# Optimization experiments

Hardware: AMD Instinct MI355X
Metric: run time of the kernel (lower is better)

## Reference

```python
import jax, jax.numpy as jnp
import numpy as np

HEADS = 32


def _conv1x1(x, w, b):
    # x: (B, Cin, H, W); w: (Cout, Cin); 1x1 conv == per-pixel GEMM
    return jnp.einsum('bchw,oc->bohw', x, w) + b[None, :, None, None]


def _grid_sample2d_zeros(value, grid):
    # value: (N, C, H, W); grid: (N, H, W, 2), normalized coords in [-1, 1],
    # grid[..., 0] = x (width axis), grid[..., 1] = y (height axis).
    # Bilinear, align_corners=True, zeros padding applied per dimension.
    N, C, H, W = value.shape
    ix = (grid[..., 0] + 1.0) * (W - 1) * 0.5
    iy = (grid[..., 1] + 1.0) * (H - 1) * 0.5
    x0 = jnp.floor(ix)
    y0 = jnp.floor(iy)
    dx = ix - x0  # (N, H, W)
    dy = iy - y0
    x0i = x0.astype(jnp.int32)
    y0i = y0.astype(jnp.int32)
    x1i = x0i + 1
    y1i = y0i + 1

    def gather(yi, xi):
        valid = ((xi >= 0) & (xi < W) & (yi >= 0) & (yi < H))
        xc = jnp.clip(xi, 0, W - 1)
        yc = jnp.clip(yi, 0, H - 1)
        g = jax.vmap(lambda v, y, x: v[:, y, x])(value, yc, xc)  # (N, C, H, W)
        return g * valid[:, None, :, :].astype(value.dtype)

    out = (gather(y0i, x0i) * ((1.0 - dx) * (1.0 - dy))[:, None]
           + gather(y0i, x1i) * (dx * (1.0 - dy))[:, None]
           + gather(y1i, x0i) * ((1.0 - dx) * dy)[:, None]
           + gather(y1i, x1i) * (dx * dy)[:, None])
    return out


def _base_grid(H, W, dtype):
    ys = jnp.linspace(-1.0, 1.0, H, dtype=dtype)
    xs = jnp.linspace(-1.0, 1.0, W, dtype=dtype)
    gy, gx = jnp.meshgrid(ys, xs, indexing='ij')
    return jnp.stack([gx, gy], axis=-1)  # (H, W, 2)


def setup_inputs() -> dict:
    key = jax.random.key(0)
    k = jax.random.split(key, 8)
    B, Cin, Cout, H, W = 4, 256, 256, 128, 128
    u = jax.random.normal(k[0], (B, Cin, H, W), dtype=jnp.float32)
    s_in = 1.0 / np.sqrt(Cin)
    s_out = 1.0 / np.sqrt(Cout)
    w1 = jax.random.normal(k[1], (Cout, Cin), dtype=jnp.float32) * s_in
    b1 = jax.random.normal(k[2], (Cout,), dtype=jnp.float32) * 0.01
    w2 = jax.random.normal(k[3], (2 * HEADS, Cout), dtype=jnp.float32) * (0.1 * s_out)
    b2 = jax.random.normal(k[4], (2 * HEADS,), dtype=jnp.float32) * 0.01
    wv = jax.random.normal(k[5], (Cout, Cin), dtype=jnp.float32) * s_in
    bv = jax.random.normal(k[6], (Cout,), dtype=jnp.float32) * 0.01
    return {"u": u, "w1": w1, "b1": b1, "w2": w2, "b2": b2, "wv": wv, "bv": bv}


def reference(u, w1, b1, w2, b2, wv, bv):
    B, Cin, H, W = u.shape
    # flow_head: 1x1 conv -> ReLU -> 1x1 conv producing n_dims*heads channels
    h = jax.nn.relu(_conv1x1(u, w1, b1))
    flow = _conv1x1(h, w2, b2)          # (B, heads*2, H, W)
    value = _conv1x1(u, wv, bv)         # (B, Cout, H, W)
    Ci = value.shape[1] // HEADS
    # 'B (heads dir) H W -> (B heads) H W dir'
    flow = flow.reshape(B, HEADS, 2, H, W).transpose(0, 1, 3, 4, 2)
    flow = flow.reshape(B * HEADS, H, W, 2)
    # 'B (heads C_i) H W -> (B heads) C_i H W'
    value = value.reshape(B * HEADS, Ci, H, W)
    grid = _base_grid(H, W, u.dtype)[None] + flow  # (B*heads, H, W, 2)
    warp = _grid_sample2d_zeros(value, grid)       # (B*heads, Ci, H, W)
    # '(B heads) C_i H W -> B (heads C_i) H W'
    return warp.reshape(B, HEADS * Ci, H, W)
```

## Files before the change

kernel.cpp:

```cpp
#include <hip/hip_runtime.h>
#include <cstddef>

#define HW 16384

typedef short s8v __attribute__((ext_vector_type(8)));
typedef short s4v __attribute__((ext_vector_type(4)));
typedef float f4v __attribute__((ext_vector_type(4)));

__device__ inline short f2b(float x) {
    union { float f; unsigned u; } v; v.f = x;
    unsigned r = v.u + 0x7fff + ((v.u >> 16) & 1);
    return (short)(r >> 16);
}
__device__ inline float b2f(short h) {
    union { unsigned u; float f; } v;
    v.u = ((unsigned)(unsigned short)h) << 16;
    return v.f;
}

__device__ inline void bar_lgkm() {
    asm volatile("s_waitcnt lgkmcnt(0)\n\ts_barrier" ::: "memory");
}

__global__ __launch_bounds__(256) void k_prep_w(
    const float* __restrict__ w1, const float* __restrict__ wv,
    const float* __restrict__ w2,
    short* __restrict__ Wthi, short* __restrict__ Wtlo,
    short* __restrict__ w2thi, short* __restrict__ w2tlo)
{
    int tid = blockIdx.x * 256 + threadIdx.x;
    if (tid < 131072) {
        int c = tid >> 14, r = tid & 16383, ch = r >> 5, kk = r & 31;
        float f = (ch < 256) ? w1[ch * 256 + c * 32 + kk]
                             : wv[(ch - 256) * 256 + c * 32 + kk];
        short hi = f2b(f);
        Wthi[tid] = hi;
        if (ch < 256) Wtlo[(c * 256 + ch) * 32 + kk] = f2b(f - b2f(hi));
    } else {
        int o = tid - 131072;
        int c = o >> 11, r = o & 2047, dir = r >> 5, kk = r & 31;
        float f = w2[dir * 256 + c * 32 + kk];
        short hi = f2b(f);
        w2thi[o] = hi;
        w2tlo[o] = f2b(f - b2f(hi));
    }
}

__global__ __launch_bounds__(256, 2) void k_mega(
    const float* __restrict__ u,
    const short* __restrict__ Wthi, const short* __restrict__ Wtlo,
    const short* __restrict__ w2thi, const short* __restrict__ w2tlo,
    const float* __restrict__ b1, const float* __restrict__ bv,
    const float* __restrict__ b2,
    unsigned short* __restrict__ vbuf, float* __restrict__ flow)
{
    __shared__ __attribute__((aligned(16))) char smem[69632];
    short* T1h = (short*)smem;
    short* T1l = T1h + 4352;
    short* T2h = (short*)(smem + 17408);
    short* T2l = T2h + 4608;
    short* vt  = (short*)smem;
    short* hhi = (short*)smem;
    short* hlo = (short*)(smem + 34816);

    const int t = threadIdx.x;
    const int l = t & 63;
    const int w = t >> 6;
    const int lr = l & 15;
    const int quad = l >> 4;
    const int quad8 = quad * 8;
    const int pt = blockIdx.x * 64;
    const int b  = pt >> 14;
    const int p0 = pt & 16383;
    const float* ub = u + (size_t)b * 256 * HW + p0;
    const int pxB = 16 * w + lr;

    f4v acc_h[4][4], acc_v[4][4];
    #pragma unroll
    for (int i = 0; i < 4; ++i)
        #pragma unroll
        for (int j = 0; j < 4; ++j) {
            acc_h[i][j] = (f4v){0.f, 0.f, 0.f, 0.f};
            acc_v[i][j] = (f4v){0.f, 0.f, 0.f, 0.f};
        }

    float4 cur[4];
    #pragma unroll
    for (int i = 0; i < 4; ++i) {
        int idx = t + 256 * i;
        int ch = idx >> 4, px4 = (idx & 15) * 4;
        cur[i] = *reinterpret_cast<const float4*>(ub + (size_t)ch * HW + px4);
    }

    s8v nx_hi, nx_v, nx_lo;
    {
        const size_t wb0 = ((size_t)(64 * w + lr)) * 32 + quad8;
        nx_hi = *reinterpret_cast<const s8v*>(Wthi + wb0);
        nx_v  = *reinterpret_cast<const s8v*>(Wthi + wb0 + 256 * 32);
        nx_lo = *reinterpret_cast<const s8v*>(Wtlo + wb0);
    }

    for (int pair = 0; pair < 4; ++pair) {
        #pragma unroll
        for (int i = 0; i < 4; ++i) {
            int idx = t + 256 * i;
            int ch = idx >> 4, px4 = (idx & 15) * 4;
            float4 v = cur[i];
            short h0 = f2b(v.x), h1 = f2b(v.y), h2 = f2b(v.z), h3 = f2b(v.w);
            s4v hv = {h0, h1, h2, h3};
            s4v lv = {f2b(v.x - b2f(h0)), f2b(v.y - b2f(h1)),
                      f2b(v.z - b2f(h2)), f2b(v.w - b2f(h3))};
            *reinterpret_cast<s4v*>(T1h + ch * 68 + px4) = hv;
            *reinterpret_cast<s4v*>(T1l + ch * 68 + px4) = lv;
        }
        bar_lgkm();
        #pragma unroll
        for (int part = 0; part < 2; ++part) {
            const short* src = part ? T1l : T1h;
            short* dst = part ? T2l : T2h;
            #pragma unroll
            for (int j = 0; j < 4; ++j) {
                int k4 = (l >> 4) + 4 * j;
                s4v v = { src[(4 * k4 + 0) * 68 + pxB],
                          src[(4 * k4 + 1) * 68 + pxB],
                          src[(4 * k4 + 2) * 68 + pxB],
                          src[(4 * k4 + 3) * 68 + pxB] };
                *reinterpret_cast<s4v*>(dst + pxB * 72 + 4 * k4) = v;
            }
        }
        bar_lgkm();
        if (pair < 3) {
            #pragma unroll
            for (int i = 0; i < 4; ++i) {
                int idx = t + 256 * i;
                int ch = idx >> 4, px4 = (idx & 15) * 4;
                cur[i] = *reinterpret_cast<const float4*>(
                    ub + (size_t)((pair + 1) * 64 + ch) * HW + px4);
            }
        }
        #pragma unroll
        for (int s = 0; s < 2; ++s) {
            int c = pair * 2 + s;
            s8v bh4[4], bl4[4];
            #pragma unroll
            for (int j = 0; j < 4; ++j) {
                bh4[j] = *reinterpret_cast<const s8v*>(T2h + (16 * j + lr) * 72 + s * 32 + quad8);
                bl4[j] = *reinterpret_cast<const s8v*>(T2l + (16 * j + lr) * 72 + s * 32 + quad8);
            }
            #pragma unroll
            for (int i = 0; i < 4; ++i) {
                s8v ahi = nx_hi, av = nx_v, alo = nx_lo;
                {
                    int idx = c * 4 + i + 1;
                    int ni = idx & 3;
                    int nc = (idx >> 2) & 7;
                    const size_t wb = ((size_t)nc * 512 + 64 * w + 16 * ni + lr) * 32 + quad8;
                    nx_hi = *reinterpret_cast<const s8v*>(Wthi + wb);
                    nx_v  = *reinterpret_cast<const s8v*>(Wthi + wb + 256 * 32);
                    nx_lo = *reinterpret_cast<const s8v*>(
                        Wtlo + ((size_t)nc * 256 + 64 * w + 16 * ni + lr) * 32 + quad8);
                }
                #pragma unroll
                for (int j = 0; j < 4; ++j) {
                    acc_h[i][j] = __builtin_amdgcn_mfma_f32_16x16x32_bf16(ahi, bh4[j], acc_h[i][j], 0, 0, 0);
                    acc_h[i][j] = __builtin_amdgcn_mfma_f32_16x16x32_bf16(ahi, bl4[j], acc_h[i][j], 0, 0, 0);
                    acc_h[i][j] = __builtin_amdgcn_mfma_f32_16x16x32_bf16(alo, bh4[j], acc_h[i][j], 0, 0, 0);
                    acc_v[i][j] = __builtin_amdgcn_mfma_f32_16x16x32_bf16(av,  bh4[j], acc_v[i][j], 0, 0, 0);
                }
            }
        }
        bar_lgkm();
    }

    #pragma unroll
    for (int i = 0; i < 4; ++i) {
        float4 bias = *reinterpret_cast<const float4*>(bv + 64 * w + 16 * i + 4 * quad);
        #pragma unroll
        for (int j = 0; j < 4; ++j) {
            int px = 16 * j + lr;
            s4v pk = { f2b(acc_v[i][j][0] + bias.x), f2b(acc_v[i][j][1] + bias.y),
                       f2b(acc_v[i][j][2] + bias.z), f2b(acc_v[i][j][3] + bias.w) };
            *reinterpret_cast<s4v*>(vt + px * 272 + 64 * w + 16 * i + 4 * quad) = pk;
        }
    }
    bar_lgkm();
    {
        int px = t >> 2;
        int h0 = (t & 3) * 8;
        size_t pix = (size_t)p0 + px;
        #pragma unroll
        for (int e = 0; e < 8; ++e) {
            int hh = h0 + e;
            s8v vv = *reinterpret_cast<const s8v*>(vt + px * 272 + hh * 8);
            *reinterpret_cast<s8v*>(
                vbuf + ((((size_t)(b * 32 + hh)) << 14) + pix) * 8) = vv;
        }
    }
    bar_lgkm();

    #pragma unroll
    for (int i = 0; i < 4; ++i) {
        float4 bias = *reinterpret_cast<const float4*>(b1 + 64 * w + 16 * i + 4 * quad);
        #pragma unroll
        for (int j = 0; j < 4; ++j) {
            int px = 16 * j + lr;
            float v0 = fmaxf(acc_h[i][j][0] + bias.x, 0.f);
            float v1 = fmaxf(acc_h[i][j][1] + bias.y, 0.f);
            float v2 = fmaxf(acc_h[i][j][2] + bias.z, 0.f);
            float v3 = fmaxf(acc_h[i][j][3] + bias.w, 0.f);
            short h0 = f2b(v0), h1 = f2b(v1), h2 = f2b(v2), h3 = f2b(v3);
            s4v hv = {h0, h1, h2, h3};
            s4v lv = {f2b(v0 - b2f(h0)), f2b(v1 - b2f(h1)),
                      f2b(v2 - b2f(h2)), f2b(v3 - b2f(h3))};
            int chb = 64 * w + 16 * i + 4 * quad;
            *reinterpret_cast<s4v*>(hhi + px * 272 + chb) = hv;
            *reinterpret_cast<s4v*>(hlo + px * 272 + chb) = lv;
        }
    }
    s8v f_hi, f_lo;
    {
        const size_t wb = ((size_t)(16 * w + lr)) * 32 + quad8;
        f_hi = *reinterpret_cast<const s8v*>(w2thi + wb);
        f_lo = *reinterpret_cast<const s8v*>(w2tlo + wb);
    }
    bar_lgkm();

    f4v acc_f[4];
    #pragma unroll
    for (int j = 0; j < 4; ++j) acc_f[j] = (f4v){0.f, 0.f, 0.f, 0.f};
    #pragma unroll
    for (int c = 0; c < 8; ++c) {
        s8v ahi = f_hi, alo = f_lo;
        {
            int ncf = (c + 1) & 7;
            const size_t wb = ((size_t)ncf * 64 + 16 * w + lr) * 32 + quad8;
            f_hi = *reinterpret_cast<const s8v*>(w2thi + wb);
            f_lo = *reinterpret_cast<const s8v*>(w2tlo + wb);
        }
        #pragma unroll
        for (int j = 0; j < 4; ++j) {
            int px = 16 * j + lr;
            s8v bhh = *reinterpret_cast<const s8v*>(hhi + px * 272 + c * 32 + quad8);
            s8v bll = *reinterpret_cast<const s8v*>(hlo + px * 272 + c * 32 + quad8);
            acc_f[j] = __builtin_amdgcn_mfma_f32_16x16x32_bf16(ahi, bhh, acc_f[j], 0, 0, 0);
            acc_f[j] = __builtin_amdgcn_mfma_f32_16x16x32_bf16(ahi, bll, acc_f[j], 0, 0, 0);
            acc_f[j] = __builtin_amdgcn_mfma_f32_16x16x32_bf16(alo, bhh, acc_f[j], 0, 0, 0);
        }
    }
    float4 b2v = *reinterpret_cast<const float4*>(b2 + 16 * w + 4 * quad);
    #pragma unroll
    for (int r = 0; r < 4; ++r) {
        int dir = 16 * w + 4 * quad + r;
        float bias = (r == 0) ? b2v.x : (r == 1) ? b2v.y : (r == 2) ? b2v.z : b2v.w;
        #pragma unroll
        for (int j = 0; j < 4; ++j)
            flow[((size_t)b * 64 + dir) * HW + p0 + 16 * j + lr] = acc_f[j][r] + bias;
    }
}

__global__ __launch_bounds__(256) void k_warp(
    const float* __restrict__ flow, const unsigned short* __restrict__ vbuf,
    float* __restrict__ out)
{
    const int g = blockIdx.x * 256 + threadIdx.x;
    const int p = g & 16383;
    const int n = g >> 14;
    const int b = n >> 5;
    const int head = n & 31;
    const int y = p >> 7;
    const int x = p & 127;

    float fx = flow[((size_t)b * 64 + 2 * head + 0) * HW + p];
    float fy = flow[((size_t)b * 64 + 2 * head + 1) * HW + p];
    float ix = (float)x + fx * 63.5f;
    float iy = (float)y + fy * 63.5f;

    float x0f = floorf(ix), y0f = floorf(iy);
    float dx = ix - x0f, dy = iy - y0f;
    int x0 = (int)x0f, y0 = (int)y0f;
    int x1 = x0 + 1,   y1 = y0 + 1;

    bool vx0 = (x0 >= 0) & (x0 < 128);
    bool vx1 = (x1 >= 0) & (x1 < 128);
    bool vy0 = (y0 >= 0) & (y0 < 128);
    bool vy1 = (y1 >= 0) & (y1 < 128);
    int x0c = min(max(x0, 0), 127), x1c = min(max(x1, 0), 127);
    int y0c = min(max(y0, 0), 127), y1c = min(max(y1, 0), 127);

    float w00 = (1.f - dx) * (1.f - dy) * ((vx0 & vy0) ? 1.f : 0.f);
    float w10 = dx * (1.f - dy)        * ((vx1 & vy0) ? 1.f : 0.f);
    float w01 = (1.f - dx) * dy        * ((vx0 & vy1) ? 1.f : 0.f);
    float w11 = dx * dy                * ((vx1 & vy1) ? 1.f : 0.f);

    const unsigned short* vb = vbuf + (((size_t)n) << 14) * 8;
    s8v v00 = *reinterpret_cast<const s8v*>(vb + (size_t)(y0c * 128 + x0c) * 8);
    s8v v10 = *reinterpret_cast<const s8v*>(vb + (size_t)(y0c * 128 + x1c) * 8);
    s8v v01 = *reinterpret_cast<const s8v*>(vb + (size_t)(y1c * 128 + x0c) * 8);
    s8v v11 = *reinterpret_cast<const s8v*>(vb + (size_t)(y1c * 128 + x1c) * 8);

    float* ob = out + ((size_t)b * 256 + head * 8) * HW + p;
    #pragma unroll
    for (int ci = 0; ci < 8; ++ci) {
        float v = w00 * b2f(v00[ci]) + w10 * b2f(v10[ci])
                + w01 * b2f(v01[ci]) + w11 * b2f(v11[ci]);
        ob[(size_t)ci * HW] = v;
    }
}

extern "C" void kernel_launch(void* const* d_in, const int* in_sizes, int n_in,
                              void* d_out, int out_size, void* d_ws, size_t ws_size,
                              hipStream_t stream) {
    const float* u  = (const float*)d_in[0];
    const float* w1 = (const float*)d_in[1];
    const float* b1 = (const float*)d_in[2];
    const float* w2 = (const float*)d_in[3];
    const float* b2 = (const float*)d_in[4];
    const float* wv = (const float*)d_in[5];
    const float* bv = (const float*)d_in[6];

    char* ws = (char*)d_ws;
    unsigned short* vbuf = (unsigned short*)ws;
    float* flow  = (float*)(ws + 33554432ull);
    short* Wthi  = (short*)(ws + 50331648ull);
    short* Wtlo  = Wthi + 131072;
    short* w2thi = Wtlo + 65536;
    short* w2tlo = w2thi + 16384;
    float* out = (float*)d_out;

    k_prep_w<<<dim3(576),  dim3(256), 0, stream>>>(w1, wv, w2, Wthi, Wtlo, w2thi, w2tlo);
    k_mega  <<<dim3(1024), dim3(256), 0, stream>>>(u, Wthi, Wtlo, w2thi, w2tlo,
                                                   b1, bv, b2, vbuf, flow);
    k_warp  <<<dim3(8192), dim3(256), 0, stream>>>(flow, vbuf, out);
}
```

Baseline: 198.0 us.

## Double-buffer LDS staging of input tiles and truncate low-part bf16 conversion

Restructures the main GEMM loop so the two LDS staging steps (fp32 to hi/lo bf16 split, then transpose) are double-buffered. The next pair's staging now overlaps with the current pair's MFMA work, which drops two of the three barriers per iteration. The low-part bf16 residual now uses truncation instead of round-to-nearest to save ALU work, giving a slight accuracy change. Shared memory rises a little and the loop is fully unrolled, which could raise register pressure against the occupancy-2 launch bound.

After: 200.2 us. No clear change (+1.1%).

```diff
diff --git a/kernel.cpp b/kernel.cpp
--- a/kernel.cpp
+++ b/kernel.cpp
@@ -11,6 +11,10 @@
     union { float f; unsigned u; } v; v.f = x;
     unsigned r = v.u + 0x7fff + ((v.u >> 16) & 1);
     return (short)(r >> 16);
+}
+__device__ inline short f2bt(float x) {
+    union { float f; unsigned u; } v; v.f = x;
+    return (short)(v.u >> 16);
 }
 __device__ inline float b2f(short h) {
     union { unsigned u; float f; } v;
@@ -54,11 +58,9 @@
     const float* __restrict__ b2,
     unsigned short* __restrict__ vbuf, float* __restrict__ flow)
 {
-    __shared__ __attribute__((aligned(16))) char smem[69632];
-    short* T1h = (short*)smem;
-    short* T1l = T1h + 4352;
-    short* T2h = (short*)(smem + 17408);
-    short* T2l = T2h + 4608;
+    __shared__ __attribute__((aligned(16))) char smem[71680];
+    short* T1 = (short*)smem;
+    short* T2 = (short*)(smem + 34816);
     short* vt  = (short*)smem;
     short* hhi = (short*)smem;
     short* hlo = (short*)(smem + 34816);
@@ -85,12 +87,49 @@
         }
 
     float4 cur[4];
-    #pragma unroll
-    for (int i = 0; i < 4; ++i) {
-        int idx = t + 256 * i;
-        int ch = idx >> 4, px4 = (idx & 15) * 4;
-        cur[i] = *reinterpret_cast<const float4*>(ub + (size_t)ch * HW + px4);
-    }
+    auto loadU = [&](int pr) {
+        #pragma unroll
+        for (int i = 0; i < 4; ++i) {
+            int idx = t + 256 * i;
+            int ch = idx >> 4, px4 = (idx & 15) * 4;
+            cur[i] = *reinterpret_cast<const float4*>(
+                ub + (size_t)(pr * 64 + ch) * HW + px4);
+        }
+    };
+    auto stageA = [&](int buf) {
+        short* th = T1 + buf * 8704;
+        short* tl = th + 4352;
+        #pragma unroll
+        for (int i = 0; i < 4; ++i) {
+            int idx = t + 256 * i;
+            int ch = idx >> 4, px4 = (idx & 15) * 4;
+            float4 v = cur[i];
+            short h0 = f2b(v.x), h1 = f2b(v.y), h2 = f2b(v.z), h3 = f2b(v.w);
+            s4v hv = {h0, h1, h2, h3};
+            s4v lv = {f2bt(v.x - b2f(h0)), f2bt(v.y - b2f(h1)),
+                      f2bt(v.z - b2f(h2)), f2bt(v.w - b2f(h3))};
+            *reinterpret_cast<s4v*>(th + ch * 68 + px4) = hv;
+            *reinterpret_cast<s4v*>(tl + ch * 68 + px4) = lv;
+        }
+    };
+    auto stageB = [&](int sbuf, int tbuf) {
+        const short* sh = T1 + sbuf * 8704;
+        short* dh = T2 + tbuf * 9216;
+        #pragma unroll
+        for (int part = 0; part < 2; ++part) {
+            const short* src = sh + part * 4352;
+            short* dst = dh + part * 4608;
+            #pragma unroll
+            for (int j = 0; j < 4; ++j) {
+                int k4 = quad + 4 * j;
+                s4v v = { src[(4 * k4 + 0) * 68 + pxB],
+                          src[(4 * k4 + 1) * 68 + pxB],
+                          src[(4 * k4 + 2) * 68 + pxB],
+                          src[(4 * k4 + 3) * 68 + pxB] };
+                *reinterpret_cast<s4v*>(dst + pxB * 72 + 4 * k4) = v;
+            }
+        }
+    };
 
     s8v nx_hi, nx_v, nx_lo;
     {
@@ -100,52 +139,28 @@
         nx_lo = *reinterpret_cast<const s8v*>(Wtlo + wb0);
     }
 
+    loadU(0);
+    stageA(0);  loadU(1);
+    bar_lgkm();
+    stageB(0, 0);
+    stageA(1);  loadU(2);
+    bar_lgkm();
+
+    #pragma unroll
     for (int pair = 0; pair < 4; ++pair) {
-        #pragma unroll
-        for (int i = 0; i < 4; ++i) {
-            int idx = t + 256 * i;
-            int ch = idx >> 4, px4 = (idx & 15) * 4;
-            float4 v = cur[i];
-            short h0 = f2b(v.x), h1 = f2b(v.y), h2 = f2b(v.z), h3 = f2b(v.w);
-            s4v hv = {h0, h1, h2, h3};
-            s4v lv = {f2b(v.x - b2f(h0)), f2b(v.y - b2f(h1)),
-                      f2b(v.z - b2f(h2)), f2b(v.w - b2f(h3))};
-            *reinterpret_cast<s4v*>(T1h + ch * 68 + px4) = hv;
-            *reinterpret_cast<s4v*>(T1l + ch * 68 + px4) = lv;
-        }
-        bar_lgkm();
-        #pragma unroll
-        for (int part = 0; part < 2; ++part) {
-            const short* src = part ? T1l : T1h;
-            short* dst = part ? T2l : T2h;
-            #pragma unroll
-            for (int j = 0; j < 4; ++j) {
-                int k4 = (l >> 4) + 4 * j;
-                s4v v = { src[(4 * k4 + 0) * 68 + pxB],
-                          src[(4 * k4 + 1) * 68 + pxB],
-                          src[(4 * k4 + 2) * 68 + pxB],
-                          src[(4 * k4 + 3) * 68 + pxB] };
-                *reinterpret_cast<s4v*>(dst + pxB * 72 + 4 * k4) = v;
-            }
-        }
-        bar_lgkm();
-        if (pair < 3) {
-            #pragma unroll
-            for (int i = 0; i < 4; ++i) {
-                int idx = t + 256 * i;
-                int ch = idx >> 4, px4 = (idx & 15) * 4;
-                cur[i] = *reinterpret_cast<const float4*>(
-                    ub + (size_t)((pair + 1) * 64 + ch) * HW + px4);
-            }
-        }
+        if (pair < 3) stageB((pair + 1) & 1, (pair + 1) & 1);
+        if (pair < 2) stageA(pair & 1);
+        if (pair == 0) loadU(3);
+        const short* T2hb = T2 + (pair & 1) * 9216;
+        const short* T2lb = T2hb + 4608;
         #pragma unroll
         for (int s = 0; s < 2; ++s) {
             int c = pair * 2 + s;
             s8v bh4[4], bl4[4];
             #pragma unroll
             for (int j = 0; j < 4; ++j) {
-                bh4[j] = *reinterpret_cast<const s8v*>(T2h + (16 * j + lr) * 72 + s * 32 + quad8);
-                bl4[j] = *reinterpret_cast<const s8v*>(T2l + (16 * j + lr) * 72 + s * 32 + quad8);
+                bh4[j] = *reinterpret_cast<const s8v*>(T2hb + (16 * j + lr) * 72 + s * 32 + quad8);
+                bl4[j] = *reinterpret_cast<const s8v*>(T2lb + (16 * j + lr) * 72 + s * 32 + quad8);
             }
             #pragma unroll
             for (int i = 0; i < 4; ++i) {
@@ -169,7 +184,7 @@
                 }
             }
         }
-        bar_lgkm();
+        if (pair < 3) bar_lgkm();
     }
 
     #pragma unroll
@@ -210,8 +225,8 @@
             float v3 = fmaxf(acc_h[i][j][3] + bias.w, 0.f);
             short h0 = f2b(v0), h1 = f2b(v1), h2 = f2b(v2), h3 = f2b(v3);
             s4v hv = {h0, h1, h2, h3};
-            s4v lv = {f2b(v0 - b2f(h0)), f2b(v1 - b2f(h1)),
-                      f2b(v2 - b2f(h2)), f2b(v3 - b2f(h3))};
+            s4v lv = {f2bt(v0 - b2f(h0)), f2bt(v1 - b2f(h1)),
+                      f2bt(v2 - b2f(h2)), f2bt(v3 - b2f(h3))};
             int chb = 64 * w + 16 * i + 4 * quad;
             *reinterpret_cast<s4v*>(hhi + px * 272 + chb) = hv;
             *reinterpret_cast<s4v*>(hlo + px * 272 + chb) = lv;
```

## Interleave flow layout, XCD-aware warp blocks, two pixels per thread, truncating lo split

Applied to the files above, without the earlier changes.

The flow buffer is rewritten as interleaved (x,y) float2 per head, so the warp kernel reads one 8-byte value instead of two separate planes. The warp kernel now handles two adjacent pixels per thread with float2 output stores. Its block index is remapped so that each XCD processes a contiguous set of heads, which keeps each head's value slab local to one L2. The low half of the bf16 hi/lo split now truncates instead of rounding to cut ALU work, at a small cost in precision; the wave quad index is also reused instead of recomputed.

Measured after the change: 191.7 us. -3.2%, faster.

```diff
diff --git a/kernel.cpp b/kernel.cpp
--- a/kernel.cpp
+++ b/kernel.cpp
@@ -11,6 +11,10 @@
     union { float f; unsigned u; } v; v.f = x;
     unsigned r = v.u + 0x7fff + ((v.u >> 16) & 1);
     return (short)(r >> 16);
+}
+__device__ inline short f2bt(float x) {
+    union { float f; unsigned u; } v; v.f = x;
+    return (short)(v.u >> 16);
 }
 __device__ inline float b2f(short h) {
     union { unsigned u; float f; } v;
@@ -108,8 +112,8 @@
             float4 v = cur[i];
             short h0 = f2b(v.x), h1 = f2b(v.y), h2 = f2b(v.z), h3 = f2b(v.w);
             s4v hv = {h0, h1, h2, h3};
-            s4v lv = {f2b(v.x - b2f(h0)), f2b(v.y - b2f(h1)),
-                      f2b(v.z - b2f(h2)), f2b(v.w - b2f(h3))};
+            s4v lv = {f2bt(v.x - b2f(h0)), f2bt(v.y - b2f(h1)),
+                      f2bt(v.z - b2f(h2)), f2bt(v.w - b2f(h3))};
             *reinterpret_cast<s4v*>(T1h + ch * 68 + px4) = hv;
             *reinterpret_cast<s4v*>(T1l + ch * 68 + px4) = lv;
         }
@@ -120,7 +124,7 @@
             short* dst = part ? T2l : T2h;
             #pragma unroll
             for (int j = 0; j < 4; ++j) {
-                int k4 = (l >> 4) + 4 * j;
+                int k4 = quad + 4 * j;
                 s4v v = { src[(4 * k4 + 0) * 68 + pxB],
                           src[(4 * k4 + 1) * 68 + pxB],
                           src[(4 * k4 + 2) * 68 + pxB],
@@ -210,8 +214,8 @@
             float v3 = fmaxf(acc_h[i][j][3] + bias.w, 0.f);
             short h0 = f2b(v0), h1 = f2b(v1), h2 = f2b(v2), h3 = f2b(v3);
             s4v hv = {h0, h1, h2, h3};
-            s4v lv = {f2b(v0 - b2f(h0)), f2b(v1 - b2f(h1)),
-                      f2b(v2 - b2f(h2)), f2b(v3 - b2f(h3))};
+            s4v lv = {f2bt(v0 - b2f(h0)), f2bt(v1 - b2f(h1)),
+                      f2bt(v2 - b2f(h2)), f2bt(v3 - b2f(h3))};
             int chb = 64 * w + 16 * i + 4 * quad;
             *reinterpret_cast<s4v*>(hhi + px * 272 + chb) = hv;
             *reinterpret_cast<s4v*>(hlo + px * 272 + chb) = lv;
@@ -248,13 +252,15 @@
         }
     }
     float4 b2v = *reinterpret_cast<const float4*>(b2 + 16 * w + 4 * quad);
-    #pragma unroll
-    for (int r = 0; r < 4; ++r) {
-        int dir = 16 * w + 4 * quad + r;
-        float bias = (r == 0) ? b2v.x : (r == 1) ? b2v.y : (r == 2) ? b2v.z : b2v.w;
-        #pragma unroll
-        for (int j = 0; j < 4; ++j)
-            flow[((size_t)b * 64 + dir) * HW + p0 + 16 * j + lr] = acc_f[j][r] + bias;
+    float2* fl2 = reinterpret_cast<float2*>(flow);
+    const int head0 = 8 * w + 2 * quad;
+    #pragma unroll
+    for (int j = 0; j < 4; ++j) {
+        int p = p0 + 16 * j + lr;
+        float2 f01 = { acc_f[j][0] + b2v.x, acc_f[j][1] + b2v.y };
+        float2 f23 = { acc_f[j][2] + b2v.z, acc_f[j][3] + b2v.w };
+        fl2[(size_t)(b * 32 + head0) * HW + p] = f01;
+        fl2[(size_t)(b * 32 + head0 + 1) * HW + p] = f23;
     }
 }
 
@@ -262,48 +268,62 @@
     const float* __restrict__ flow, const unsigned short* __restrict__ vbuf,
     float* __restrict__ out)
 {
-    const int g = blockIdx.x * 256 + threadIdx.x;
-    const int p = g & 16383;
-    const int n = g >> 14;
+    const int bid = blockIdx.x;
+    const int xcd = bid & 7;
+    const int idx = bid >> 3;
+    const int n   = xcd * 16 + (idx >> 5);
+    const int blk = idx & 31;
+    const int p   = (blk << 9) + (threadIdx.x << 1);
     const int b = n >> 5;
     const int head = n & 31;
-    const int y = p >> 7;
-    const int x = p & 127;
-
-    float fx = flow[((size_t)b * 64 + 2 * head + 0) * HW + p];
-    float fy = flow[((size_t)b * 64 + 2 * head + 1) * HW + p];
-    float ix = (float)x + fx * 63.5f;
-    float iy = (float)y + fy * 63.5f;
-
-    float x0f = floorf(ix), y0f = floorf(iy);
-    float dx = ix - x0f, dy = iy - y0f;
-    int x0 = (int)x0f, y0 = (int)y0f;
-    int x1 = x0 + 1,   y1 = y0 + 1;
-
-    bool vx0 = (x0 >= 0) & (x0 < 128);
-    bool vx1 = (x1 >= 0) & (x1 < 128);
-    bool vy0 = (y0 >= 0) & (y0 < 128);
-    bool vy1 = (y1 >= 0) & (y1 < 128);
-    int x0c = min(max(x0, 0), 127), x1c = min(max(x1, 0), 127);
-    int y0c = min(max(y0, 0), 127), y1c = min(max(y1, 0), 127);
-
-    float w00 = (1.f - dx) * (1.f - dy) * ((vx0 & vy0) ? 1.f : 0.f);
-    float w10 = dx * (1.f - dy)        * ((vx1 & vy0) ? 1.f : 0.f);
-    float w01 = (1.f - dx) * dy        * ((vx0 & vy1) ? 1.f : 0.f);
-    float w11 = dx * dy                * ((vx1 & vy1) ? 1.f : 0.f);
-
+
+    const float2* fl2 = reinterpret_cast<const float2*>(flow) + (size_t)n * HW;
     const unsigned short* vb = vbuf + (((size_t)n) << 14) * 8;
-    s8v v00 = *reinterpret_cast<const s8v*>(vb + (size_t)(y0c * 128 + x0c) * 8);
-    s8v v10 = *reinterpret_cast<const s8v*>(vb + (size_t)(y0c * 128 + x1c) * 8);
-    s8v v01 = *reinterpret_cast<const s8v*>(vb + (size_t)(y1c * 128 + x0c) * 8);
-    s8v v11 = *reinterpret_cast<const s8v*>(vb + (size_t)(y1c * 128 + x1c) * 8);
+
+    float vals[8][2];
+    #pragma unroll
+    for (int e = 0; e < 2; ++e) {
+        int pp = p + e;
+        int y = pp >> 7;
+        int x = pp & 127;
+        float2 fv = fl2[pp];
+        float ix = (float)x + fv.x * 63.5f;
+        float iy = (float)y + fv.y * 63.5f;
+
+        float x0f = floorf(ix), y0f = floorf(iy);
+        float dx = ix - x0f, dy = iy - y0f;
+        int x0 = (int)x0f, y0 = (int)y0f;
+        int x1 = x0 + 1,   y1 = y0 + 1;
+
+        bool vx0 = (x0 >= 0) & (x0 < 128);
+        bool vx1 = (x1 >= 0) & (x1 < 128);
+        bool vy0 = (y0 >= 0) & (y0 < 128);
+        bool vy1 = (y1 >= 0) & (y1 < 128);
+        int x0c = min(max(x0, 0), 127), x1c = min(max(x1, 0), 127);
+        int y0c = min(max(y0, 0), 127), y1c = min(max(y1, 0), 127);
+
+        float w00 = (1.f - dx) * (1.f - dy) * ((vx0 & vy0) ? 1.f : 0.f);
+        float w10 = dx * (1.f - dy)        * ((vx1 & vy0) ? 1.f : 0.f);
+        float w01 = (1.f - dx) * dy        * ((vx0 & vy1) ? 1.f : 0.f);
+        float w11 = dx * dy                * ((vx1 & vy1) ? 1.f : 0.f);
+
+        s8v v00 = *reinterpret_cast<const s8v*>(vb + (size_t)(y0c * 128 + x0c) * 8);
+        s8v v10 = *reinterpret_cast<const s8v*>(vb + (size_t)(y0c * 128 + x1c) * 8);
+        s8v v01 = *reinterpret_cast<const s8v*>(vb + (size_t)(y1c * 128 + x0c) * 8);
+        s8v v11 = *reinterpret_cast<const s8v*>(vb + (size_t)(y1c * 128 + x1c) * 8);
+
+        #pragma unroll
+        for (int ci = 0; ci < 8; ++ci) {
+            vals[ci][e] = w00 * b2f(v00[ci]) + w10 * b2f(v10[ci])
+                        + w01 * b2f(v01[ci]) + w11 * b2f(v11[ci]);
+        }
+    }
 
     float* ob = out + ((size_t)b * 256 + head * 8) * HW + p;
     #pragma unroll
     for (int ci = 0; ci < 8; ++ci) {
-        float v = w00 * b2f(v00[ci]) + w10 * b2f(v10[ci])
-                + w01 * b2f(v01[ci]) + w11 * b2f(v11[ci]);
-        ob[(size_t)ci * HW] = v;
+        float2 o2 = { vals[ci][0], vals[ci][1] };
+        *reinterpret_cast<float2*>(ob + (size_t)ci * HW) = o2;
     }
 }
 
@@ -330,5 +350,5 @@
     k_prep_w<<<dim3(576),  dim3(256), 0, stream>>>(w1, wv, w2, Wthi, Wtlo, w2thi, w2tlo);
     k_mega  <<<dim3(1024), dim3(256), 0, stream>>>(u, Wthi, Wtlo, w2thi, w2tlo,
                                                    b1, bv, b2, vbuf, flow);
-    k_warp  <<<dim3(8192), dim3(256), 0, stream>>>(flow, vbuf, out);
-}
+    k_warp  <<<dim3(4096), dim3(256), 0, stream>>>(flow, vbuf, out);
+}
```
